# Optimization experiments

Hardware: AMD Instinct MI355X
Metric: run time of the kernel (lower is better)

The kernel has to match this reference:

```python
import jax, jax.numpy as jnp
import numpy as np

B, N, ZDIM = 8, 2048, 128
NPOINTS = 32
BN_EPS = 1e-5


def setup_inputs() -> dict:
    key = jax.random.key(0)
    ks = iter(jax.random.split(key, 64))

    def w(shape, s=0.05):
        return jax.random.normal(next(ks), shape, jnp.float32) * s

    inp = {"x": jax.random.normal(next(ks), (B, N, 3), jnp.float32)}
    inp.update(dict(
        w1=w((128, 3)), b1=w((128,)),
        w2=w((128, 128)), b2=w((128,)),
        w3=w((256, 128)), b3=w((256,)),
        w4=w((512, 256)), b4=w((512,)),
        a1_wqk=w((32, 1)), a1_wt=w((128, 128)), a1_bt=w((128,)),
        a2_wqk=w((32, 1)), a2_wt=w((128, 128)), a2_bt=w((128,)),
        a3_wqk=w((64, 1)), a3_wt=w((256, 256)), a3_bt=w((256,)),
        a4_wqk=w((128, 1)), a4_wt=w((512, 512)), a4_bt=w((512,)),
        fc1m_w=w((256, 512)), fc1m_b=w((256,)),
        fc2m_w=w((128, 256)), fc2m_b=w((128,)),
        fc3m_w=w((ZDIM, 128)), fc3m_b=w((ZDIM,)),
        fc1v_w=w((256, 512)), fc1v_b=w((256,)),
        fc2v_w=w((128, 256)), fc2v_b=w((128,)),
        fc3v_w=w((1, 128)), fc3v_b=w((1,)),
    ))
    return inp


def bn_cn(h):
    # BatchNorm1d over [B, C, N] features (training-mode batch stats, affine=identity at init)
    m = h.mean(axis=(0, 2), keepdims=True)
    v = h.var(axis=(0, 2), keepdims=True)
    return (h - m) * jax.lax.rsqrt(v + BN_EPS)


def bn_f(h):
    # BatchNorm1d over [B, F]
    m = h.mean(axis=0, keepdims=True)
    v = h.var(axis=0, keepdims=True)
    return (h - m) * jax.lax.rsqrt(v + BN_EPS)


def conv1x1(h, w, b):
    # 1x1 Conv1d: [B,Cin,N] x [Cout,Cin] -> [B,Cout,N]
    return jnp.einsum('oc,bcn->bon', w, h) + b[None, :, None]


def angle_density(xyz):
    # xyz: [B,N,3]; 1 - cosine similarity between all point pairs (computed as GEMM,
    # never materializing the [B,N,N,3] expanded tensors of the torch code)
    xn = xyz / jnp.linalg.norm(xyz, axis=-1, keepdims=True)
    dist = 1.0 - jnp.einsum('bnc,bmc->bnm', xn, xn)  # [B,N,N]
    neg_vals, _ = jax.lax.top_k(-dist, NPOINTS)       # 32 smallest distances
    feat_density = (-neg_vals).mean(axis=-1)          # [B,N]
    inv = 1.0 / feat_density
    return inv / jnp.max(inv)


def density_attn(h, dens, wqk, wt, bt):
    # h: [B,C,N], dens: [B,1,N]; q_conv and k_conv share weights
    q = jnp.einsum('dc,bcn->bdn', wqk, dens)          # [B,D4,N]
    energy = jnp.einsum('bdn,bdm->bnm', q, q)         # [B,N,N]
    attn = jax.nn.softmax(energy, axis=-1)
    attn = attn / (1e-9 + attn.sum(axis=1, keepdims=True))
    x_r = jnp.einsum('bcn,bnm->bcm', h, attn)         # [B,C,N]
    t = conv1x1(h - x_r, wt, bt)
    t = jax.nn.relu(bn_cn(t))
    return h + t


def reference(x, w1, b1, w2, b2, w3, b3, w4, b4,
              a1_wqk, a1_wt, a1_bt, a2_wqk, a2_wt, a2_bt,
              a3_wqk, a3_wt, a3_bt, a4_wqk, a4_wt, a4_bt,
              fc1m_w, fc1m_b, fc2m_w, fc2m_b, fc3m_w, fc3m_b,
              fc1v_w, fc1v_b, fc2v_w, fc2v_b, fc3v_w, fc3v_b):
    dens = angle_density(x)[:, None, :]               # [B,1,N]
    h = jnp.swapaxes(x, 1, 2)                         # [B,3,N]
    h = jax.nn.relu(bn_cn(conv1x1(h, w1, b1)))
    h = density_attn(h, dens, a1_wqk, a1_wt, a1_bt)
    h = jax.nn.relu(bn_cn(conv1x1(h, w2, b2)))
    h = density_attn(h, dens, a2_wqk, a2_wt, a2_bt)
    h = jax.nn.relu(bn_cn(conv1x1(h, w3, b3)))
    h = density_attn(h, dens, a3_wqk, a3_wt, a3_bt)
    h = bn_cn(conv1x1(h, w4, b4))                     # no relu on conv4 (matches source)
    h = density_attn(h, dens, a4_wqk, a4_wt, a4_bt)
    g = jnp.max(h, axis=2)                            # [B,512] global max pool

    u = jax.nn.relu(bn_f(g @ fc1m_w.T + fc1m_b))
    u = jax.nn.relu(bn_f(u @ fc2m_w.T + fc2m_b))
    u = u @ fc3m_w.T + fc3m_b
    u = u / jnp.linalg.norm(u, axis=-1, keepdims=True)

    k = jax.nn.relu(bn_f(g @ fc1v_w.T + fc1v_b))
    k = jax.nn.relu(bn_f(k @ fc2v_w.T + fc2v_b))
    k = k @ fc3v_w.T + fc3v_b
    k = jax.nn.softplus(k) + 1.0
    return (u, k)
```

## Files before the change

kernel.cpp:

```cpp
#include <hip/hip_runtime.h>
#include <cfloat>
#include <cmath>

constexpr int NB = 8;
constexpr int NP = 2048;
constexpr int NK = 11;

typedef __attribute__((ext_vector_type(4))) float f32x4;
typedef __attribute__((ext_vector_type(8))) short bf16x8;
#define MFMA16(a, b, c) __builtin_amdgcn_mfma_f32_16x16x32_bf16(a, b, c, 0, 0, 0)

__device__ inline ushort f2bf(float f) {
  union { float f; unsigned u; } v; v.f = f;
  unsigned r = v.u + 0x7FFFu + ((v.u >> 16) & 1u);
  return (ushort)(r >> 16);
}
__device__ inline unsigned pk2bf(float a, float b) {
  return (unsigned)f2bf(a) | ((unsigned)f2bf(b) << 16);
}

__device__ inline int dpp_half_sum_i32(int c) {
  c += __builtin_amdgcn_update_dpp(0, c, 0x111, 0xf, 0xf, true);
  c += __builtin_amdgcn_update_dpp(0, c, 0x112, 0xf, 0xf, true);
  c += __builtin_amdgcn_update_dpp(0, c, 0x114, 0xf, 0xf, true);
  c += __builtin_amdgcn_update_dpp(0, c, 0x118, 0xf, 0xf, true);
  c += __builtin_amdgcn_update_dpp(0, c, 0x142, 0xf, 0xf, true);
  return c;
}

__global__ void k_prep(const float* __restrict__ x, float* __restrict__ xn, float* __restrict__ xt) {
  int i = blockIdx.x * blockDim.x + threadIdx.x;
  if (i >= NB * NP) return;
  int b = i >> 11, n = i & (NP - 1);
  float a0 = x[i * 3 + 0], a1 = x[i * 3 + 1], a2 = x[i * 3 + 2];
  float rn = rsqrtf(a0 * a0 + a1 * a1 + a2 * a2);
  xn[i * 3 + 0] = a0 * rn; xn[i * 3 + 1] = a1 * rn; xn[i * 3 + 2] = a2 * rn;
  float* xb = xt + (size_t)b * 3 * NP;
  xb[0 * NP + n] = a0; xb[1 * NP + n] = a1; xb[2 * NP + n] = a2;
}

__global__ void k_zero1(float* p) { if (threadIdx.x == 0) p[0] = 0.f; }

__global__ __launch_bounds__(512, 1) void k_density(const float* __restrict__ xn,
                                                    float* __restrict__ inv,
                                                    int* __restrict__ maxinv) {
  __shared__ float sx[NP], sy[NP], sz[NP];
  int t = threadIdx.x;
  int w = t >> 6, lane = t & 63, half = lane >> 5, sl = lane & 31;
  int row0 = blockIdx.x * 16;
  int b = row0 >> 11;
  const float4* xb4 = (const float4*)(xn + (size_t)b * NP * 3);
  {
    float4 a = xb4[t * 3 + 0], c4 = xb4[t * 3 + 1], e4 = xb4[t * 3 + 2];
    int p = t * 4;
    sx[p + 0] = a.x;  sy[p + 0] = a.y;  sz[p + 0] = a.z;
    sx[p + 1] = a.w;  sy[p + 1] = c4.x; sz[p + 1] = c4.y;
    sx[p + 2] = c4.z; sy[p + 2] = c4.w; sz[p + 2] = e4.x;
    sx[p + 3] = e4.y; sy[p + 3] = e4.z; sz[p + 3] = e4.w;
  }
  __syncthreads();
  int row = row0 + w * 2 + half;
  int n = row & (NP - 1);
  float px = sx[n], py = sy[n], pz = sz[n];
  float d[64];
  float mn = FLT_MAX, mx = -FLT_MAX;
  #pragma unroll
  for (int k = 0; k < 64; ++k) {
    int m = sl + (k << 5);
    float v = 1.0f - (px * sx[m] + py * sy[m] + pz * sz[m]);
    d[k] = v;
    mn = fminf(mn, v); mx = fmaxf(mx, v);
  }
  #pragma unroll
  for (int off = 16; off; off >>= 1) {
    mn = fminf(mn, __shfl_xor(mn, off));
    mx = fminf(mx, __shfl_xor(mx, off));
  }
  float lo = mn, hi = mx + 1e-6f;
  int baddr = (half ? 63 : 31) << 2;
  for (int it = 0; it < 7; ++it) {
    float dd = hi - lo;
    float t1 = lo + 0.25f * dd, t2 = lo + 0.5f * dd, t3 = lo + 0.75f * dd;
    int c12 = 0, c3 = 0;
    #pragma unroll
    for (int k = 0; k < 64; ++k) {
      float v = d[k];
      c12 += (v < t1 ? 1 : 0) + (v < t2 ? 65536 : 0);
      c3  += (v < t3 ? 1 : 0);
    }
    c12 = dpp_half_sum_i32(c12);
    c3  = dpp_half_sum_i32(c3);
    c12 = __builtin_amdgcn_ds_bpermute(baddr, c12);
    c3  = __builtin_amdgcn_ds_bpermute(baddr, c3);
    int c1 = c12 & 0xFFFF, c2 = (int)(((unsigned)c12) >> 16);
    bool le3 = c3 <= 32, le2 = c2 <= 32, le1 = c1 <= 32;
    float nlo = le3 ? t3 : (le2 ? t2 : (le1 ? t1 : lo));
    float nhi = le3 ? hi : (le2 ? t3 : (le1 ? t2 : t1));
    lo = nlo; hi = nhi;
  }
  {
    float tt = 0.5f * (lo + hi);
    int c = 0;
    #pragma unroll
    for (int k = 0; k < 64; ++k) c += (d[k] < tt) ? 1 : 0;
    c = dpp_half_sum_i32(c);
    c = __builtin_amdgcn_ds_bpermute(baddr, c);
    bool le = c <= 32;
    lo = le ? tt : lo;
  }
  float s = 0.f; int c = 0;
  #pragma unroll
  for (int k = 0; k < 64; ++k) {
    bool p = d[k] < lo;
    s += p ? d[k] : 0.f;
    c += p ? 1 : 0;
  }
  c = dpp_half_sum_i32(c);
  int ctot = __builtin_amdgcn_ds_bpermute(baddr, c);
  #pragma unroll
  for (int off = 16; off; off >>= 1) s += __shfl_xor(s, off);
  float sum = s + (float)(32 - ctot) * lo;
  if (sl == 0) {
    float iv = 32.0f / sum;
    inv[row] = iv;
    atomicMax(maxinv, __float_as_int(iv));
  }
}

__global__ void k_scale(float* __restrict__ dens, const float* __restrict__ maxinv) {
  int i = blockIdx.x * 256 + threadIdx.x;
  if (i < NB * NP) dens[i] *= (1.0f / maxinv[0]);
}

__global__ __launch_bounds__(256) void k_attn_small(const float* __restrict__ dens,
                                                    const float* __restrict__ wqk, int D,
                                                    float* __restrict__ coef_out,
                                                    float* __restrict__ rinv,
                                                    float* __restrict__ cinv) {
  int b = blockIdx.x, t = threadIdx.x, w = t >> 6, lane = t & 63;
  float sv = 0.f;
  for (int i = lane; i < D; i += 64) sv += wqk[i] * wqk[i];
  #pragma unroll
  for (int off = 32; off; off >>= 1) sv += __shfl_xor(sv, off);
  float coef[NK];
  coef[0] = 1.f;
  {
    float cc = 1.f;
    #pragma unroll
    for (int k = 1; k < NK; ++k) { cc *= sv / (float)k; coef[k] = cc; }
  }
  if (b == 0 && t == 0) {
    for (int k = 0; k < NK; ++k) coef_out[k] = coef[k];
  }
  const float* db = dens + b * NP;
  float d[8], r[8];
  *(float4*)&d[0] = *(const float4*)(db + t * 8);
  *(float4*)&d[4] = *(const float4*)(db + t * 8 + 4);
  __shared__ float part[NK][4];
  float q[NK];
  {
    float acc[NK];
    #pragma unroll
    for (int k = 0; k < NK; ++k) acc[k] = 0.f;
    #pragma unroll
    for (int e = 0; e < 8; ++e) {
      float p = 1.f;
      #pragma unroll
      for (int k = 0; k < NK; ++k) { acc[k] += p; p *= d[e]; }
    }
    #pragma unroll
    for (int k = 0; k < NK; ++k) {
      float a = acc[k];
      #pragma unroll
      for (int off = 32; off; off >>= 1) a += __shfl_xor(a, off);
      if (lane == 0) part[k][w] = a;
    }
    __syncthreads();
    #pragma unroll
    for (int k = 0; k < NK; ++k)
      q[k] = coef[k] * ((part[k][0] + part[k][1]) + (part[k][2] + part[k][3]));
    __syncthreads();
  }
  #pragma unroll
  for (int e = 0; e < 8; ++e) {
    float poly = q[NK - 1];
    #pragma unroll
    for (int k = NK - 2; k >= 0; --k) poly = poly * d[e] + q[k];
    r[e] = 1.0f / poly;
  }
  *(float4*)(rinv + b * NP + t * 8)     = *(float4*)&r[0];
  *(float4*)(rinv + b * NP + t * 8 + 4) = *(float4*)&r[4];
  {
    float acc[NK];
    #pragma unroll
    for (int k = 0; k < NK; ++k) acc[k] = 0.f;
    #pragma unroll
    for (int e = 0; e < 8; ++e) {
      float p = r[e];
      #pragma unroll
      for (int k = 0; k < NK; ++k) { acc[k] += p; p *= d[e]; }
    }
    #pragma unroll
    for (int k = 0; k < NK; ++k) {
      float a = acc[k];
      #pragma unroll
      for (int off = 32; off; off >>= 1) a += __shfl_xor(a, off);
      if (lane == 0) part[k][w] = a;
    }
    __syncthreads();
    #pragma unroll
    for (int k = 0; k < NK; ++k)
      q[k] = coef[k] * ((part[k][0] + part[k][1]) + (part[k][2] + part[k][3]));
  }
  #pragma unroll
  for (int e = 0; e < 8; ++e) {
    float poly = q[NK - 1];
    #pragma unroll
    for (int k = NK - 2; k >= 0; --k) poly = poly * d[e] + q[k];
    r[e] = 1.0f / (poly + 1e-9f);
  }
  *(float4*)(cinv + b * NP + t * 8)     = *(float4*)&r[0];
  *(float4*)(cinv + b * NP + t * 8 + 4) = *(float4*)&r[4];
}

__global__ __launch_bounds__(256) void k_xrP(const float* __restrict__ H, float* __restrict__ U,
                                             const float* __restrict__ dens,
                                             const float* __restrict__ rinv,
                                             const float* __restrict__ cinv,
                                             const float* __restrict__ coef, int C) {
  int b = blockIdx.y, c = blockIdx.x, t = threadIdx.x, w = t >> 6, lane = t & 63;
  const float* Hc = H + ((size_t)b * C + c) * NP;
  float* Uc = U + ((size_t)b * C + c) * NP;
  const float* db = dens + b * NP;
  const float* rb = rinv + b * NP;
  const float* cb = cinv + b * NP;
  float h[8], d[8], r[8], cv[8];
  *(float4*)&h[0] = *(const float4*)(Hc + t * 8);
  *(float4*)&h[4] = *(const float4*)(Hc + t * 8 + 4);
  *(float4*)&d[0] = *(const float4*)(db + t * 8);
  *(float4*)&d[4] = *(const float4*)(db + t * 8 + 4);
  *(float4*)&r[0] = *(const float4*)(rb + t * 8);
  *(float4*)&r[4] = *(const float4*)(rb + t * 8 + 4);
  *(float4*)&cv[0] = *(const float4*)(cb + t * 8);
  *(float4*)&cv[4] = *(const float4*)(cb + t * 8 + 4);
  float acc[NK];
  #pragma unroll
  for (int k = 0; k < NK; ++k) acc[k] = 0.f;
  #pragma unroll
  for (int e = 0; e < 8; ++e) {
    float p = h[e] * r[e];
    #pragma unroll
    for (int k = 0; k < NK; ++k) { acc[k] += p; p *= d[e]; }
  }
  __shared__ float part[NK][4];
  #pragma unroll
  for (int k = 0; k < NK; ++k) {
    float a = acc[k];
    #pragma unroll
    for (int off = 32; off; off >>= 1) a += __shfl_xor(a, off);
    if (lane == 0) part[k][w] = a;
  }
  __syncthreads();
  float q[NK];
  #pragma unroll
  for (int k = 0; k < NK; ++k)
    q[k] = coef[k] * ((part[k][0] + part[k][1]) + (part[k][2] + part[k][3]));
  float u[8];
  #pragma unroll
  for (int e = 0; e < 8; ++e) {
    float poly = q[NK - 1];
    #pragma unroll
    for (int k = NK - 2; k >= 0; --k) poly = poly * d[e] + q[k];
    u[e] = h[e] - cv[e] * poly;
  }
  *(float4*)(Uc + t * 8)     = *(float4*)&u[0];
  *(float4*)(Uc + t * 8 + 4) = *(float4*)&u[4];
}

constexpr int LDA = 72;

__global__ __launch_bounds__(256) void k_gemm_mfma(const float* __restrict__ W,
                                                   const float* __restrict__ IN,
                                                   const float* __restrict__ bias,
                                                   float* __restrict__ OUT,
                                                   int Cin, int Cout) {
  int b = blockIdx.z, n0 = blockIdx.x * 128, o0 = blockIdx.y * 128;
  int tid = threadIdx.x, lane = tid & 63, w = tid >> 6;
  int wr = w >> 1, wc = w & 1;
  const float* Ib = IN + (size_t)b * Cin * NP;
  float* Ob = OUT + (size_t)b * Cout * NP;
  __shared__ ushort Asm[128 * LDA];
  __shared__ ushort Bsm[128 * LDA];
  f32x4 acc[4][4];
  #pragma unroll
  for (int i = 0; i < 4; ++i)
    #pragma unroll
    for (int j = 0; j < 4; ++j) acc[i][j] = (f32x4)(0.0f);

  int row = tid >> 1, half = tid & 1;
  int csub = tid & 63, q = tid >> 6;
  for (int cc0 = 0; cc0 < Cin; cc0 += 64) {
    __syncthreads();
    {
      const float* src = W + (size_t)(o0 + row) * Cin + cc0 + half * 32;
      unsigned* dst = (unsigned*)(Asm + row * LDA + half * 32);
      #pragma unroll
      for (int i = 0; i < 8; ++i) {
        float4 v = *(const float4*)(src + i * 4);
        dst[i * 2 + 0] = pk2bf(v.x, v.y);
        dst[i * 2 + 1] = pk2bf(v.z, v.w);
      }
      const float* isrc = Ib + (size_t)(cc0 + csub) * NP + n0 + q * 32;
      #pragma unroll
      for (int i = 0; i < 8; ++i) {
        float4 v = *(const float4*)(isrc + i * 4);
        ushort* bd = Bsm + (q * 32 + i * 4) * LDA + csub;
        bd[0]       = f2bf(v.x);
        bd[LDA]     = f2bf(v.y);
        bd[2 * LDA] = f2bf(v.z);
        bd[3 * LDA] = f2bf(v.w);
      }
    }
    __syncthreads();
    #pragma unroll
    for (int kk = 0; kk < 64; kk += 32) {
      bf16x8 af[4], bfr[4];
      #pragma unroll
      for (int i = 0; i < 4; ++i) {
        af[i]  = *(const bf16x8*)(Asm + (wr * 64 + i * 16 + (lane & 15)) * LDA + kk + (lane >> 4) * 8);
        bfr[i] = *(const bf16x8*)(Bsm + (wc * 64 + i * 16 + (lane & 15)) * LDA + kk + (lane >> 4) * 8);
      }
      #pragma unroll
      for (int i = 0; i < 4; ++i)
        #pragma unroll
        for (int j = 0; j < 4; ++j)
          acc[i][j] = MFMA16(af[i], bfr[j], acc[i][j]);
    }
  }
  #pragma unroll
  for (int i = 0; i < 4; ++i) {
    #pragma unroll
    for (int r = 0; r < 4; ++r) {
      int o = o0 + wr * 64 + i * 16 + (lane >> 4) * 4 + r;
      float bv = bias[o];
      #pragma unroll
      for (int j = 0; j < 4; ++j) {
        int n = n0 + wc * 64 + j * 16 + (lane & 15);
        Ob[(size_t)o * NP + n] = acc[i][j][r] + bv;
      }
    }
  }
}

__global__ __launch_bounds__(256) void k_gemm(const float* __restrict__ W,
                                              const float* __restrict__ IN,
                                              const float* __restrict__ bias,
                                              float* __restrict__ OUT,
                                              int Cin, int Cout) {
  int b = blockIdx.z;
  int n0 = blockIdx.x * 64;
  int o0 = blockIdx.y * 64;
  int tid = threadIdx.x;
  int tx = tid & 15, ty = tid >> 4;
  const float* Ib = IN + (size_t)b * Cin * NP;
  float* Ob = OUT + (size_t)b * Cout * NP;
  __shared__ float Wt[64][65];
  __shared__ float It[64][65];
  float acc[4][4] = {};
  for (int c0 = 0; c0 < Cin; c0 += 64) {
    __syncthreads();
    {
      int ci = tid & 63, ob4 = tid >> 6;
      bool cv = (c0 + ci) < Cin;
      #pragma unroll
      for (int k = 0; k < 16; ++k) {
        int oi = ob4 + (k << 2);
        Wt[ci][oi] = cv ? W[(size_t)(o0 + oi) * Cin + c0 + ci] : 0.f;
      }
      int ni = tid & 63, cb4 = tid >> 6;
      #pragma unroll
      for (int k = 0; k < 16; ++k) {
        int ci2 = cb4 + (k << 2);
        It[ci2][ni] = (c0 + ci2) < Cin ? Ib[(size_t)(c0 + ci2) * NP + n0 + ni] : 0.f;
      }
    }
    __syncthreads();
    #pragma unroll 4
    for (int ci = 0; ci < 64; ++ci) {
      float a0 = Wt[ci][ty * 4 + 0], a1 = Wt[ci][ty * 4 + 1], a2 = Wt[ci][ty * 4 + 2], a3 = Wt[ci][ty * 4 + 3];
      float b0 = It[ci][tx * 4 + 0], b1 = It[ci][tx * 4 + 1], b2 = It[ci][tx * 4 + 2], b3 = It[ci][tx * 4 + 3];
      acc[0][0] += a0 * b0; acc[0][1] += a0 * b1; acc[0][2] += a0 * b2; acc[0][3] += a0 * b3;
      acc[1][0] += a1 * b0; acc[1][1] += a1 * b1; acc[1][2] += a1 * b2; acc[1][3] += a1 * b3;
      acc[2][0] += a2 * b0; acc[2][1] += a2 * b1; acc[2][2] += a2 * b2; acc[2][3] += a2 * b3;
      acc[3][0] += a3 * b0; acc[3][1] += a3 * b1; acc[3][2] += a3 * b2; acc[3][3] += a3 * b3;
    }
  }
  #pragma unroll
  for (int i = 0; i < 4; ++i) {
    int o = o0 + ty * 4 + i;
    float bv = bias[o];
    #pragma unroll
    for (int j = 0; j < 4; ++j) {
      int n = n0 + tx * 4 + j;
      Ob[(size_t)o * NP + n] = acc[i][j] + bv;
    }
  }
}

__global__ __launch_bounds__(256) void k_bn(const float* __restrict__ T, float* __restrict__ H,
                                            int C, int relu, int acc, int pool,
                                            float* __restrict__ gout) {
  int c = blockIdx.x, t = threadIdx.x, w = t >> 6, lane = t & 63;
  float4 v[16];
  float s = 0.f, s2 = 0.f;
  #pragma unroll
  for (int b = 0; b < NB; ++b) {
    const float4* p = (const float4*)(T + ((size_t)b * C + c) * NP);
    #pragma unroll
    for (int i = 0; i < 2; ++i) {
      float4 x = p[t + i * 256];
      v[b * 2 + i] = x;
      s += (x.x + x.y) + (x.z + x.w);
      s2 += (x.x * x.x + x.y * x.y) + (x.z * x.z + x.w * x.w);
    }
  }
  #pragma unroll
  for (int off = 32; off; off >>= 1) { s += __shfl_xor(s, off); s2 += __shfl_xor(s2, off); }
  __shared__ float ps[4], ps2[4];
  if (lane == 0) { ps[w] = s; ps2[w] = s2; }
  __syncthreads();
  float ts = (ps[0] + ps[1]) + (ps[2] + ps[3]);
  float ts2 = (ps2[0] + ps2[1]) + (ps2[2] + ps2[3]);
  float m = ts * (1.0f / (NB * NP));
  float var = ts2 * (1.0f / (NB * NP)) - m * m;
  float is = rsqrtf(var + 1e-5f);
  float bmax[NB];
  #pragma unroll
  for (int b = 0; b < NB; ++b) bmax[b] = -FLT_MAX;
  #pragma unroll
  for (int b = 0; b < NB; ++b) {
    float4* hp = (float4*)(H + ((size_t)b * C + c) * NP);
    #pragma unroll
    for (int i = 0; i < 2; ++i) {
      float4 x = v[b * 2 + i];
      x.x = (x.x - m) * is; x.y = (x.y - m) * is; x.z = (x.z - m) * is; x.w = (x.w - m) * is;
      if (relu) {
        x.x = fmaxf(x.x, 0.f); x.y = fmaxf(x.y, 0.f); x.z = fmaxf(x.z, 0.f); x.w = fmaxf(x.w, 0.f);
      }
      if (acc) {
        float4 h = hp[t + i * 256];
        x.x += h.x; x.y += h.y; x.z += h.z; x.w += h.w;
      }
      hp[t + i * 256] = x;
      if (pool) bmax[b] = fmaxf(bmax[b], fmaxf(fmaxf(x.x, x.y), fmaxf(x.z, x.w)));
    }
  }
  if (pool) {
    __shared__ float pm[4][NB];
    #pragma unroll
    for (int b = 0; b < NB; ++b) {
      float m2 = bmax[b];
      #pragma unroll
      for (int off = 32; off; off >>= 1) m2 = fmaxf(m2, __shfl_xor(m2, off));
      if (lane == 0) pm[w][b] = m2;
    }
    __syncthreads();
    if (t < NB) {
      float m2 = fmaxf(fmaxf(pm[0][t], pm[1][t]), fmaxf(pm[2][t], pm[3][t]));
      gout[t * C + c] = m2;
    }
  }
}

__global__ __launch_bounds__(256) void k_head(const float* __restrict__ g,
    const float* __restrict__ f1mw, const float* __restrict__ f1mb,
    const float* __restrict__ f2mw, const float* __restrict__ f2mb,
    const float* __restrict__ f3mw, const float* __restrict__ f3mb,
    const float* __restrict__ f1vw, const float* __restrict__ f1vb,
    const float* __restrict__ f2vw, const float* __restrict__ f2vb,
    const float* __restrict__ f3vw, const float* __restrict__ f3vb,
    float* __restrict__ out) {
  bool vpath = (blockIdx.x == 1);
  const float* w1 = vpath ? f1vw : f1mw;
  const float* c1 = vpath ? f1vb : f1mb;
  const float* w2 = vpath ? f2vw : f2mw;
  const float* c2 = vpath ? f2vb : f2mb;
  __shared__ float gg[NB * 512];
  __shared__ float a1[NB * 256];
  __shared__ float a2[NB * 128];
  __shared__ float zz[NB * 128];
  __shared__ float nrm[NB];
  int t = threadIdx.x;
  for (int i = t; i < NB * 512; i += 256) gg[i] = g[i];
  __syncthreads();
  float o[NB];
  {
    #pragma unroll
    for (int b = 0; b < NB; ++b) o[b] = c1[t];
    const float* wr = w1 + (size_t)t * 512;
    for (int j = 0; j < 512; ++j) {
      float w = wr[j];
      #pragma unroll
      for (int b = 0; b < NB; ++b) o[b] += gg[b * 512 + j] * w;
    }
    float mean = 0.f;
    #pragma unroll
    for (int b = 0; b < NB; ++b) mean += o[b];
    mean *= (1.0f / NB);
    float var = 0.f;
    #pragma unroll
    for (int b = 0; b < NB; ++b) { float d = o[b] - mean; var += d * d; }
    var *= (1.0f / NB);
    float is = rsqrtf(var + 1e-5f);
    #pragma unroll
    for (int b = 0; b < NB; ++b) a1[b * 256 + t] = fmaxf((o[b] - mean) * is, 0.f);
  }
  __syncthreads();
  if (t < 128) {
    #pragma unroll
    for (int b = 0; b < NB; ++b) o[b] = c2[t];
    const float* wr = w2 + (size_t)t * 256;
    for (int j = 0; j < 256; ++j) {
      float w = wr[j];
      #pragma unroll
      for (int b = 0; b < NB; ++b) o[b] += a1[b * 256 + j] * w;
    }
    float mean = 0.f;
    #pragma unroll
    for (int b = 0; b < NB; ++b) mean += o[b];
    mean *= (1.0f / NB);
    float var = 0.f;
    #pragma unroll
    for (int b = 0; b < NB; ++b) { float d = o[b] - mean; var += d * d; }
    var *= (1.0f / NB);
    float is = rsqrtf(var + 1e-5f);
    #pragma unroll
    for (int b = 0; b < NB; ++b) a2[b * 128 + t] = fmaxf((o[b] - mean) * is, 0.f);
  }
  __syncthreads();
  if (!vpath) {
    if (t < 128) {
      const float* wr = f3mw + (size_t)t * 128;
      for (int b = 0; b < NB; ++b) {
        float s = f3mb[t];
        for (int j = 0; j < 128; ++j) s += a2[b * 128 + j] * wr[j];
        zz[b * 128 + t] = s;
      }
    }
    __syncthreads();
    if (t < NB) {
      float s = 0.f;
      for (int j = 0; j < 128; ++j) { float v = zz[t * 128 + j]; s += v * v; }
      nrm[t] = sqrtf(s);
    }
    __syncthreads();
    if (t < 128) {
      for (int b = 0; b < NB; ++b) out[b * 128 + t] = zz[b * 128 + t] / nrm[b];
    }
  } else {
    if (t < NB) {
      float s = f3vb[0];
      for (int j = 0; j < 128; ++j) s += a2[t * 128 + j] * f3vw[j];
      float sp = (s > 20.f) ? s : log1pf(expf(s));
      out[NB * 128 + t] = sp + 1.0f;
    }
  }
}

extern "C" void kernel_launch(void* const* d_in, const int* in_sizes, int n_in,
                              void* d_out, int out_size, void* d_ws, size_t ws_size,
                              hipStream_t stream) {
  const float* x  = (const float*)d_in[0];
  const float* w1 = (const float*)d_in[1];
  const float* b1 = (const float*)d_in[2];
  const float* w2 = (const float*)d_in[3];
  const float* b2 = (const float*)d_in[4];
  const float* w3 = (const float*)d_in[5];
  const float* b3 = (const float*)d_in[6];
  const float* w4 = (const float*)d_in[7];
  const float* b4 = (const float*)d_in[8];
  const float* a_wqk[4] = {(const float*)d_in[9],  (const float*)d_in[12], (const float*)d_in[15], (const float*)d_in[18]};
  const float* a_wt[4]  = {(const float*)d_in[10], (const float*)d_in[13], (const float*)d_in[16], (const float*)d_in[19]};
  const float* a_bt[4]  = {(const float*)d_in[11], (const float*)d_in[14], (const float*)d_in[17], (const float*)d_in[20]};
  int a_D[4] = {in_sizes[9], in_sizes[12], in_sizes[15], in_sizes[18]};
  const float* f1mw = (const float*)d_in[21]; const float* f1mb = (const float*)d_in[22];
  const float* f2mw = (const float*)d_in[23]; const float* f2mb = (const float*)d_in[24];
  const float* f3mw = (const float*)d_in[25]; const float* f3mb = (const float*)d_in[26];
  const float* f1vw = (const float*)d_in[27]; const float* f1vb = (const float*)d_in[28];
  const float* f2vw = (const float*)d_in[29]; const float* f2vb = (const float*)d_in[30];
  const float* f3vw = (const float*)d_in[31]; const float* f3vb = (const float*)d_in[32];
  float* out = (float*)d_out;

  float* ws = (float*)d_ws;
  float* xn     = ws; ws += (size_t)NB * NP * 3;
  float* dens   = ws; ws += NB * NP;
  float* maxinv = ws; ws += 16;
  float* coef   = ws; ws += 16;
  float* rinv   = ws; ws += NB * NP;
  float* cinv   = ws; ws += NB * NP;
  float* g      = ws; ws += NB * 512;
  float* Hb     = ws; ws += (size_t)NB * 512 * NP;
  float* Ub     = ws; ws += (size_t)NB * 512 * NP;
  float* Tb     = ws; ws += (size_t)NB * 512 * NP;

  k_prep<<<NB * NP / 256, 256, 0, stream>>>(x, xn, Ub);
  k_zero1<<<1, 64, 0, stream>>>(maxinv);
  k_density<<<NB * NP / 16, 512, 0, stream>>>(xn, dens, (int*)maxinv);
  k_scale<<<NB * NP / 256, 256, 0, stream>>>(dens, maxinv);

  auto conv = [&](const float* W, const float* bias, const float* IN, int Cin, int Cout, bool relu) {
    if (Cin < 64)
      k_gemm<<<dim3(NP / 64, Cout / 64, NB), 256, 0, stream>>>(W, IN, bias, Tb, Cin, Cout);
    else
      k_gemm_mfma<<<dim3(NP / 128, Cout / 128, NB), 256, 0, stream>>>(W, IN, bias, Tb, Cin, Cout);
    k_bn<<<Cout, 256, 0, stream>>>(Tb, Hb, Cout, relu ? 1 : 0, 0, 0, g);
  };
  auto attn = [&](int li, int C) {
    k_attn_small<<<NB, 256, 0, stream>>>(dens, a_wqk[li], a_D[li], coef, rinv, cinv);
    k_xrP<<<dim3(C, NB), 256, 0, stream>>>(Hb, Ub, dens, rinv, cinv, coef, C);
    k_gemm_mfma<<<dim3(NP / 128, C / 128, NB), 256, 0, stream>>>(a_wt[li], Ub, a_bt[li], Tb, C, C);
    k_bn<<<C, 256, 0, stream>>>(Tb, Hb, C, 1, 1, (li == 3) ? 1 : 0, g);
  };

  conv(w1, b1, Ub, 3, 128, true);
  attn(0, 128);
  conv(w2, b2, Hb, 128, 128, true);
  attn(1, 128);
  conv(w3, b3, Hb, 128, 256, true);
  attn(2, 256);
  conv(w4, b4, Hb, 256, 512, false);
  attn(3, 512);

  k_head<<<2, 256, 0, stream>>>(g, f1mw, f1mb, f2mw, f2mb, f3mw, f3mb,
                                f1vw, f1vb, f2vw, f2vb, f3vw, f3vb, out);
}
```

Measured before the change: 467.8 us.

## Store density distances as fp16 in LDS and bisect on integer bit patterns

The density top-k kernel now gives each row a full wavefront, keeps its 2048 distances as packed fp16 in shared memory instead of 64 fp32 registers per lane, and bisects on the integer fp16 bit patterns using whole-wave DPP reductions. The aim is to cut register pressure so more blocks fit per CU, and to make the threshold search exact over a discrete range. The cost is more LDS traffic per search pass, twice as many blocks, and fp16 rounding of the distances, which may change the selected threshold and sum slightly.

```diff
diff --git a/kernel.cpp b/kernel.cpp
--- a/kernel.cpp
+++ b/kernel.cpp
@@ -1,4 +1,5 @@
 #include <hip/hip_runtime.h>
+#include <hip/hip_fp16.h>
 #include <cfloat>
 #include <cmath>
 
@@ -19,13 +20,14 @@
   return (unsigned)f2bf(a) | ((unsigned)f2bf(b) << 16);
 }
 
-__device__ inline int dpp_half_sum_i32(int c) {
+__device__ inline int dpp_wave_sum_i32(int c) {
   c += __builtin_amdgcn_update_dpp(0, c, 0x111, 0xf, 0xf, true);
   c += __builtin_amdgcn_update_dpp(0, c, 0x112, 0xf, 0xf, true);
   c += __builtin_amdgcn_update_dpp(0, c, 0x114, 0xf, 0xf, true);
   c += __builtin_amdgcn_update_dpp(0, c, 0x118, 0xf, 0xf, true);
   c += __builtin_amdgcn_update_dpp(0, c, 0x142, 0xf, 0xf, true);
-  return c;
+  c += __builtin_amdgcn_update_dpp(0, c, 0x143, 0xf, 0xf, true);
+  return __builtin_amdgcn_readlane(c, 63);
 }
 
 __global__ void k_prep(const float* __restrict__ x, float* __restrict__ xn, float* __restrict__ xt) {
@@ -41,13 +43,14 @@
 
 __global__ void k_zero1(float* p) { if (threadIdx.x == 0) p[0] = 0.f; }
 
-__global__ __launch_bounds__(512, 1) void k_density(const float* __restrict__ xn,
-                                                    float* __restrict__ inv,
-                                                    int* __restrict__ maxinv) {
+__global__ __launch_bounds__(512) void k_density(const float* __restrict__ xn,
+                                                 float* __restrict__ inv,
+                                                 int* __restrict__ maxinv) {
   __shared__ float sx[NP], sy[NP], sz[NP];
+  __shared__ uint2 dq[8][NP / 4];
   int t = threadIdx.x;
-  int w = t >> 6, lane = t & 63, half = lane >> 5, sl = lane & 31;
-  int row0 = blockIdx.x * 16;
+  int w = t >> 6, lane = t & 63;
+  int row0 = blockIdx.x * 8;
   int b = row0 >> 11;
   const float4* xb4 = (const float4*)(xn + (size_t)b * NP * 3);
   {
@@ -59,68 +62,82 @@
     sx[p + 3] = e4.y; sy[p + 3] = e4.z; sz[p + 3] = e4.w;
   }
   __syncthreads();
-  int row = row0 + w * 2 + half;
+  int row = row0 + w;
   int n = row & (NP - 1);
   float px = sx[n], py = sy[n], pz = sz[n];
-  float d[64];
-  float mn = FLT_MAX, mx = -FLT_MAX;
-  #pragma unroll
-  for (int k = 0; k < 64; ++k) {
-    int m = sl + (k << 5);
-    float v = 1.0f - (px * sx[m] + py * sy[m] + pz * sz[m]);
-    d[k] = v;
-    mn = fminf(mn, v); mx = fmaxf(mx, v);
-  }
-  #pragma unroll
-  for (int off = 16; off; off >>= 1) {
-    mn = fminf(mn, __shfl_xor(mn, off));
-    mx = fminf(mx, __shfl_xor(mx, off));
-  }
-  float lo = mn, hi = mx + 1e-6f;
-  int baddr = (half ? 63 : 31) << 2;
-  for (int it = 0; it < 7; ++it) {
-    float dd = hi - lo;
-    float t1 = lo + 0.25f * dd, t2 = lo + 0.5f * dd, t3 = lo + 0.75f * dd;
+  uint2* drow = dq[w];
+  int mni = 0xFFFF, mxi = 0;
+  #pragma unroll
+  for (int k4 = 0; k4 < 8; ++k4) {
+    unsigned u[4];
+    #pragma unroll
+    for (int i = 0; i < 4; ++i) {
+      int m = lane + ((k4 * 4 + i) << 6);
+      float v = fmaxf(1.0f - (px * sx[m] + py * sy[m] + pz * sz[m]), 0.0f);
+      u[i] = (unsigned)__half_as_ushort(__float2half(v));
+      mni = min(mni, (int)u[i]); mxi = max(mxi, (int)u[i]);
+    }
+    drow[(k4 << 6) + lane] = make_uint2(u[0] | (u[1] << 16), u[2] | (u[3] << 16));
+  }
+  #pragma unroll
+  for (int off = 32; off; off >>= 1) {
+    mni = min(mni, __shfl_xor(mni, off));
+    mxi = min(mxi, __shfl_xor(mxi, off));
+  }
+  int lo = mni, hi = mxi + 1;
+  #pragma unroll
+  for (int it = 0; it < 8; ++it) {
+    int dd = hi - lo;
+    int t1 = lo + (dd >> 2), t2 = lo + (dd >> 1), t3 = lo + dd - (dd >> 2);
     int c12 = 0, c3 = 0;
     #pragma unroll
-    for (int k = 0; k < 64; ++k) {
-      float v = d[k];
-      c12 += (v < t1 ? 1 : 0) + (v < t2 ? 65536 : 0);
-      c3  += (v < t3 ? 1 : 0);
-    }
-    c12 = dpp_half_sum_i32(c12);
-    c3  = dpp_half_sum_i32(c3);
-    c12 = __builtin_amdgcn_ds_bpermute(baddr, c12);
-    c3  = __builtin_amdgcn_ds_bpermute(baddr, c3);
+    for (int k4 = 0; k4 < 8; ++k4) {
+      uint2 pp = drow[(k4 << 6) + lane];
+      int e0 = (int)(pp.x & 0xFFFF), e1 = (int)(pp.x >> 16);
+      int e2 = (int)(pp.y & 0xFFFF), e3 = (int)(pp.y >> 16);
+      int a1 = (e0 < t1 ? 1 : 0) + (e1 < t1 ? 1 : 0) + (e2 < t1 ? 1 : 0) + (e3 < t1 ? 1 : 0);
+      int a2 = (e0 < t2 ? 1 : 0) + (e1 < t2 ? 1 : 0) + (e2 < t2 ? 1 : 0) + (e3 < t2 ? 1 : 0);
+      c12 += a1 + (a2 << 16);
+      c3  += (e0 < t3 ? 1 : 0) + (e1 < t3 ? 1 : 0) + (e2 < t3 ? 1 : 0) + (e3 < t3 ? 1 : 0);
+    }
+    c12 = dpp_wave_sum_i32(c12);
+    c3  = dpp_wave_sum_i32(c3);
     int c1 = c12 & 0xFFFF, c2 = (int)(((unsigned)c12) >> 16);
     bool le3 = c3 <= 32, le2 = c2 <= 32, le1 = c1 <= 32;
-    float nlo = le3 ? t3 : (le2 ? t2 : (le1 ? t1 : lo));
-    float nhi = le3 ? hi : (le2 ? t3 : (le1 ? t2 : t1));
+    int nlo = le3 ? t3 : (le2 ? t2 : (le1 ? t1 : lo));
+    int nhi = le3 ? hi : (le2 ? t3 : (le1 ? t2 : t1));
     lo = nlo; hi = nhi;
   }
-  {
-    float tt = 0.5f * (lo + hi);
+  #pragma unroll
+  for (int it = 0; it < 2; ++it) {
+    int tt = lo + ((hi - lo) >> 1);
     int c = 0;
     #pragma unroll
-    for (int k = 0; k < 64; ++k) c += (d[k] < tt) ? 1 : 0;
-    c = dpp_half_sum_i32(c);
-    c = __builtin_amdgcn_ds_bpermute(baddr, c);
-    bool le = c <= 32;
-    lo = le ? tt : lo;
+    for (int k4 = 0; k4 < 8; ++k4) {
+      uint2 pp = drow[(k4 << 6) + lane];
+      c += ((int)(pp.x & 0xFFFF) < tt ? 1 : 0) + ((int)(pp.x >> 16) < tt ? 1 : 0)
+         + ((int)(pp.y & 0xFFFF) < tt ? 1 : 0) + ((int)(pp.y >> 16) < tt ? 1 : 0);
+    }
+    c = dpp_wave_sum_i32(c);
+    if (c <= 32) lo = tt; else hi = tt;
   }
   float s = 0.f; int c = 0;
   #pragma unroll
-  for (int k = 0; k < 64; ++k) {
-    bool p = d[k] < lo;
-    s += p ? d[k] : 0.f;
-    c += p ? 1 : 0;
-  }
-  c = dpp_half_sum_i32(c);
-  int ctot = __builtin_amdgcn_ds_bpermute(baddr, c);
-  #pragma unroll
-  for (int off = 16; off; off >>= 1) s += __shfl_xor(s, off);
-  float sum = s + (float)(32 - ctot) * lo;
-  if (sl == 0) {
+  for (int k4 = 0; k4 < 8; ++k4) {
+    uint2 pp = drow[(k4 << 6) + lane];
+    int e[4] = {(int)(pp.x & 0xFFFF), (int)(pp.x >> 16), (int)(pp.y & 0xFFFF), (int)(pp.y >> 16)};
+    #pragma unroll
+    for (int i = 0; i < 4; ++i) {
+      bool p = e[i] < lo;
+      s += p ? __half2float(__ushort_as_half((ushort)e[i])) : 0.f;
+      c += p ? 1 : 0;
+    }
+  }
+  int ctot = dpp_wave_sum_i32(c);
+  #pragma unroll
+  for (int off = 32; off; off >>= 1) s += __shfl_xor(s, off);
+  float sum = s + (float)(32 - ctot) * __half2float(__ushort_as_half((ushort)lo));
+  if (lane == 0) {
     float iv = 32.0f / sum;
     inv[row] = iv;
     atomicMax(maxinv, __float_as_int(iv));
@@ -605,7 +622,7 @@
 
   k_prep<<<NB * NP / 256, 256, 0, stream>>>(x, xn, Ub);
   k_zero1<<<1, 64, 0, stream>>>(maxinv);
-  k_density<<<NB * NP / 16, 512, 0, stream>>>(xn, dens, (int*)maxinv);
+  k_density<<<NB * NP / 8, 512, 0, stream>>>(xn, dens, (int*)maxinv);
   k_scale<<<NB * NP / 256, 256, 0, stream>>>(dens, maxinv);
 
   auto conv = [&](const float* W, const float* bias, const float* IN, int Cin, int Cout, bool relu) {
```

Measured after the change: 554.2 us. +18.5%, slower.

## Fuse per-batch attention normalizer into k_xrP and simplify density bisection

Applied to the files above, without the earlier changes.

Removes the separate k_attn_small launch by recomputing the per-batch row and column normalizers inside every k_xrP block, so the rinv/cinv/coef buffers are no longer written or read. This saves four kernel launches and the global round-trips, at the cost of redundant polynomial reductions in every channel block (C times per batch). Separately, the top-k threshold search replaces 7 quaternary bisection steps (three thresholds each) plus one refinement with 18 plain binary bisection steps, which trades fewer compares per step for more sequential steps.

```diff
diff --git a/kernel.cpp b/kernel.cpp
--- a/kernel.cpp
+++ b/kernel.cpp
@@ -78,35 +78,16 @@
   }
   float lo = mn, hi = mx + 1e-6f;
   int baddr = (half ? 63 : 31) << 2;
-  for (int it = 0; it < 7; ++it) {
-    float dd = hi - lo;
-    float t1 = lo + 0.25f * dd, t2 = lo + 0.5f * dd, t3 = lo + 0.75f * dd;
-    int c12 = 0, c3 = 0;
-    #pragma unroll
-    for (int k = 0; k < 64; ++k) {
-      float v = d[k];
-      c12 += (v < t1 ? 1 : 0) + (v < t2 ? 65536 : 0);
-      c3  += (v < t3 ? 1 : 0);
-    }
-    c12 = dpp_half_sum_i32(c12);
-    c3  = dpp_half_sum_i32(c3);
-    c12 = __builtin_amdgcn_ds_bpermute(baddr, c12);
-    c3  = __builtin_amdgcn_ds_bpermute(baddr, c3);
-    int c1 = c12 & 0xFFFF, c2 = (int)(((unsigned)c12) >> 16);
-    bool le3 = c3 <= 32, le2 = c2 <= 32, le1 = c1 <= 32;
-    float nlo = le3 ? t3 : (le2 ? t2 : (le1 ? t1 : lo));
-    float nhi = le3 ? hi : (le2 ? t3 : (le1 ? t2 : t1));
-    lo = nlo; hi = nhi;
-  }
-  {
+  for (int it = 0; it < 18; ++it) {
     float tt = 0.5f * (lo + hi);
     int c = 0;
     #pragma unroll
     for (int k = 0; k < 64; ++k) c += (d[k] < tt) ? 1 : 0;
     c = dpp_half_sum_i32(c);
-    c = __builtin_amdgcn_ds_bpermute(baddr, c);
-    bool le = c <= 32;
+    int ct = __builtin_amdgcn_ds_bpermute(baddr, c);
+    bool le = ct <= 32;
     lo = le ? tt : lo;
+    hi = le ? hi : tt;
   }
   float s = 0.f; int c = 0;
   #pragma unroll
@@ -132,12 +113,10 @@
   if (i < NB * NP) dens[i] *= (1.0f / maxinv[0]);
 }
 
-__global__ __launch_bounds__(256) void k_attn_small(const float* __restrict__ dens,
-                                                    const float* __restrict__ wqk, int D,
-                                                    float* __restrict__ coef_out,
-                                                    float* __restrict__ rinv,
-                                                    float* __restrict__ cinv) {
-  int b = blockIdx.x, t = threadIdx.x, w = t >> 6, lane = t & 63;
+__global__ __launch_bounds__(256) void k_xrP(const float* __restrict__ H, float* __restrict__ U,
+                                             const float* __restrict__ dens,
+                                             const float* __restrict__ wqk, int D, int C) {
+  int b = blockIdx.y, c = blockIdx.x, t = threadIdx.x, w = t >> 6, lane = t & 63;
   float sv = 0.f;
   for (int i = lane; i < D; i += 64) sv += wqk[i] * wqk[i];
   #pragma unroll
@@ -149,101 +128,71 @@
     #pragma unroll
     for (int k = 1; k < NK; ++k) { cc *= sv / (float)k; coef[k] = cc; }
   }
-  if (b == 0 && t == 0) {
-    for (int k = 0; k < NK; ++k) coef_out[k] = coef[k];
-  }
-  const float* db = dens + b * NP;
-  float d[8], r[8];
-  *(float4*)&d[0] = *(const float4*)(db + t * 8);
-  *(float4*)&d[4] = *(const float4*)(db + t * 8 + 4);
-  __shared__ float part[NK][4];
-  float q[NK];
-  {
-    float acc[NK];
-    #pragma unroll
-    for (int k = 0; k < NK; ++k) acc[k] = 0.f;
-    #pragma unroll
-    for (int e = 0; e < 8; ++e) {
-      float p = 1.f;
-      #pragma unroll
-      for (int k = 0; k < NK; ++k) { acc[k] += p; p *= d[e]; }
-    }
-    #pragma unroll
-    for (int k = 0; k < NK; ++k) {
-      float a = acc[k];
-      #pragma unroll
-      for (int off = 32; off; off >>= 1) a += __shfl_xor(a, off);
-      if (lane == 0) part[k][w] = a;
-    }
-    __syncthreads();
-    #pragma unroll
-    for (int k = 0; k < NK; ++k)
-      q[k] = coef[k] * ((part[k][0] + part[k][1]) + (part[k][2] + part[k][3]));
-    __syncthreads();
-  }
-  #pragma unroll
-  for (int e = 0; e < 8; ++e) {
-    float poly = q[NK - 1];
-    #pragma unroll
-    for (int k = NK - 2; k >= 0; --k) poly = poly * d[e] + q[k];
-    r[e] = 1.0f / poly;
-  }
-  *(float4*)(rinv + b * NP + t * 8)     = *(float4*)&r[0];
-  *(float4*)(rinv + b * NP + t * 8 + 4) = *(float4*)&r[4];
-  {
-    float acc[NK];
-    #pragma unroll
-    for (int k = 0; k < NK; ++k) acc[k] = 0.f;
-    #pragma unroll
-    for (int e = 0; e < 8; ++e) {
-      float p = r[e];
-      #pragma unroll
-      for (int k = 0; k < NK; ++k) { acc[k] += p; p *= d[e]; }
-    }
-    #pragma unroll
-    for (int k = 0; k < NK; ++k) {
-      float a = acc[k];
-      #pragma unroll
-      for (int off = 32; off; off >>= 1) a += __shfl_xor(a, off);
-      if (lane == 0) part[k][w] = a;
-    }
-    __syncthreads();
-    #pragma unroll
-    for (int k = 0; k < NK; ++k)
-      q[k] = coef[k] * ((part[k][0] + part[k][1]) + (part[k][2] + part[k][3]));
-  }
-  #pragma unroll
-  for (int e = 0; e < 8; ++e) {
-    float poly = q[NK - 1];
-    #pragma unroll
-    for (int k = NK - 2; k >= 0; --k) poly = poly * d[e] + q[k];
-    r[e] = 1.0f / (poly + 1e-9f);
-  }
-  *(float4*)(cinv + b * NP + t * 8)     = *(float4*)&r[0];
-  *(float4*)(cinv + b * NP + t * 8 + 4) = *(float4*)&r[4];
-}
-
-__global__ __launch_bounds__(256) void k_xrP(const float* __restrict__ H, float* __restrict__ U,
-                                             const float* __restrict__ dens,
-                                             const float* __restrict__ rinv,
-                                             const float* __restrict__ cinv,
-                                             const float* __restrict__ coef, int C) {
-  int b = blockIdx.y, c = blockIdx.x, t = threadIdx.x, w = t >> 6, lane = t & 63;
   const float* Hc = H + ((size_t)b * C + c) * NP;
   float* Uc = U + ((size_t)b * C + c) * NP;
   const float* db = dens + b * NP;
-  const float* rb = rinv + b * NP;
-  const float* cb = cinv + b * NP;
-  float h[8], d[8], r[8], cv[8];
+  float h[8], d[8], r[8];
   *(float4*)&h[0] = *(const float4*)(Hc + t * 8);
   *(float4*)&h[4] = *(const float4*)(Hc + t * 8 + 4);
   *(float4*)&d[0] = *(const float4*)(db + t * 8);
   *(float4*)&d[4] = *(const float4*)(db + t * 8 + 4);
-  *(float4*)&r[0] = *(const float4*)(rb + t * 8);
-  *(float4*)&r[4] = *(const float4*)(rb + t * 8 + 4);
-  *(float4*)&cv[0] = *(const float4*)(cb + t * 8);
-  *(float4*)&cv[4] = *(const float4*)(cb + t * 8 + 4);
-  float acc[NK];
+  __shared__ float part[NK][4];
+  float q[NK], acc[NK];
+  #pragma unroll
+  for (int k = 0; k < NK; ++k) acc[k] = 0.f;
+  #pragma unroll
+  for (int e = 0; e < 8; ++e) {
+    float p = 1.f;
+    #pragma unroll
+    for (int k = 0; k < NK; ++k) { acc[k] += p; p *= d[e]; }
+  }
+  #pragma unroll
+  for (int k = 0; k < NK; ++k) {
+    float a = acc[k];
+    #pragma unroll
+    for (int off = 32; off; off >>= 1) a += __shfl_xor(a, off);
+    if (lane == 0) part[k][w] = a;
+  }
+  __syncthreads();
+  #pragma unroll
+  for (int k = 0; k < NK; ++k)
+    q[k] = coef[k] * ((part[k][0] + part[k][1]) + (part[k][2] + part[k][3]));
+  __syncthreads();
+  #pragma unroll
+  for (int e = 0; e < 8; ++e) {
+    float poly = q[NK - 1];
+    #pragma unroll
+    for (int k = NK - 2; k >= 0; --k) poly = poly * d[e] + q[k];
+    r[e] = 1.0f / poly;
+  }
+  #pragma unroll
+  for (int k = 0; k < NK; ++k) acc[k] = 0.f;
+  #pragma unroll
+  for (int e = 0; e < 8; ++e) {
+    float p = r[e];
+    #pragma unroll
+    for (int k = 0; k < NK; ++k) { acc[k] += p; p *= d[e]; }
+  }
+  #pragma unroll
+  for (int k = 0; k < NK; ++k) {
+    float a = acc[k];
+    #pragma unroll
+    for (int off = 32; off; off >>= 1) a += __shfl_xor(a, off);
+    if (lane == 0) part[k][w] = a;
+  }
+  __syncthreads();
+  #pragma unroll
+  for (int k = 0; k < NK; ++k)
+    q[k] = coef[k] * ((part[k][0] + part[k][1]) + (part[k][2] + part[k][3]));
+  __syncthreads();
+  float cv[8];
+  #pragma unroll
+  for (int e = 0; e < 8; ++e) {
+    float poly = q[NK - 1];
+    #pragma unroll
+    for (int k = NK - 2; k >= 0; --k) poly = poly * d[e] + q[k];
+    cv[e] = 1.0f / (poly + 1e-9f);
+  }
   #pragma unroll
   for (int k = 0; k < NK; ++k) acc[k] = 0.f;
   #pragma unroll
@@ -252,7 +201,6 @@
     #pragma unroll
     for (int k = 0; k < NK; ++k) { acc[k] += p; p *= d[e]; }
   }
-  __shared__ float part[NK][4];
   #pragma unroll
   for (int k = 0; k < NK; ++k) {
     float a = acc[k];
@@ -261,7 +209,6 @@
     if (lane == 0) part[k][w] = a;
   }
   __syncthreads();
-  float q[NK];
   #pragma unroll
   for (int k = 0; k < NK; ++k)
     q[k] = coef[k] * ((part[k][0] + part[k][1]) + (part[k][2] + part[k][3]));
@@ -595,9 +542,6 @@
   float* xn     = ws; ws += (size_t)NB * NP * 3;
   float* dens   = ws; ws += NB * NP;
   float* maxinv = ws; ws += 16;
-  float* coef   = ws; ws += 16;
-  float* rinv   = ws; ws += NB * NP;
-  float* cinv   = ws; ws += NB * NP;
   float* g      = ws; ws += NB * 512;
   float* Hb     = ws; ws += (size_t)NB * 512 * NP;
   float* Ub     = ws; ws += (size_t)NB * 512 * NP;
@@ -616,8 +560,7 @@
     k_bn<<<Cout, 256, 0, stream>>>(Tb, Hb, Cout, relu ? 1 : 0, 0, 0, g);
   };
   auto attn = [&](int li, int C) {
-    k_attn_small<<<NB, 256, 0, stream>>>(dens, a_wqk[li], a_D[li], coef, rinv, cinv);
-    k_xrP<<<dim3(C, NB), 256, 0, stream>>>(Hb, Ub, dens, rinv, cinv, coef, C);
+    k_xrP<<<dim3(C, NB), 256, 0, stream>>>(Hb, Ub, dens, a_wqk[li], a_D[li], C);
     k_gemm_mfma<<<dim3(NP / 128, C / 128, NB), 256, 0, stream>>>(a_wt[li], Ub, a_bt[li], Tb, C, C);
     k_bn<<<C, 256, 0, stream>>>(Tb, Hb, C, 1, 1, (li == 3) ? 1 : 0, g);
   };
```

After: 503.8 us. 1.08x slower.

## Fuse batchnorm with attention projection kernel and simplify density bisection

Applied to the files above, without the earlier changes.

Merges the batchnorm kernel after each conv with the density-attention x·r·P projection, so the normalized activations stay in registers and the separate k_xrP kernel no longer re-reads H from global memory. k_attn_small is moved ahead of the conv GEMM so its coefficients are ready for the fused kernel. The density top-k threshold search swaps the 7-round 4-way split for 18 rounds of plain bisection, which costs more counting passes but does one comparison per element per round. The fused kernel runs the per-batch reductions serially with a barrier each iteration, which lowers parallelism per channel.

```diff
diff --git a/kernel.cpp b/kernel.cpp
--- a/kernel.cpp
+++ b/kernel.cpp
@@ -78,35 +78,16 @@
   }
   float lo = mn, hi = mx + 1e-6f;
   int baddr = (half ? 63 : 31) << 2;
-  for (int it = 0; it < 7; ++it) {
-    float dd = hi - lo;
-    float t1 = lo + 0.25f * dd, t2 = lo + 0.5f * dd, t3 = lo + 0.75f * dd;
-    int c12 = 0, c3 = 0;
-    #pragma unroll
-    for (int k = 0; k < 64; ++k) {
-      float v = d[k];
-      c12 += (v < t1 ? 1 : 0) + (v < t2 ? 65536 : 0);
-      c3  += (v < t3 ? 1 : 0);
-    }
-    c12 = dpp_half_sum_i32(c12);
-    c3  = dpp_half_sum_i32(c3);
-    c12 = __builtin_amdgcn_ds_bpermute(baddr, c12);
-    c3  = __builtin_amdgcn_ds_bpermute(baddr, c3);
-    int c1 = c12 & 0xFFFF, c2 = (int)(((unsigned)c12) >> 16);
-    bool le3 = c3 <= 32, le2 = c2 <= 32, le1 = c1 <= 32;
-    float nlo = le3 ? t3 : (le2 ? t2 : (le1 ? t1 : lo));
-    float nhi = le3 ? hi : (le2 ? t3 : (le1 ? t2 : t1));
-    lo = nlo; hi = nhi;
-  }
-  {
+  for (int it = 0; it < 18; ++it) {
     float tt = 0.5f * (lo + hi);
     int c = 0;
     #pragma unroll
     for (int k = 0; k < 64; ++k) c += (d[k] < tt) ? 1 : 0;
     c = dpp_half_sum_i32(c);
-    c = __builtin_amdgcn_ds_bpermute(baddr, c);
-    bool le = c <= 32;
+    int ct = __builtin_amdgcn_ds_bpermute(baddr, c);
+    bool le = ct <= 32;
     lo = le ? tt : lo;
+    hi = le ? hi : tt;
   }
   float s = 0.f; int c = 0;
   #pragma unroll
@@ -221,60 +202,6 @@
   }
   *(float4*)(cinv + b * NP + t * 8)     = *(float4*)&r[0];
   *(float4*)(cinv + b * NP + t * 8 + 4) = *(float4*)&r[4];
-}
-
-__global__ __launch_bounds__(256) void k_xrP(const float* __restrict__ H, float* __restrict__ U,
-                                             const float* __restrict__ dens,
-                                             const float* __restrict__ rinv,
-                                             const float* __restrict__ cinv,
-                                             const float* __restrict__ coef, int C) {
-  int b = blockIdx.y, c = blockIdx.x, t = threadIdx.x, w = t >> 6, lane = t & 63;
-  const float* Hc = H + ((size_t)b * C + c) * NP;
-  float* Uc = U + ((size_t)b * C + c) * NP;
-  const float* db = dens + b * NP;
-  const float* rb = rinv + b * NP;
-  const float* cb = cinv + b * NP;
-  float h[8], d[8], r[8], cv[8];
-  *(float4*)&h[0] = *(const float4*)(Hc + t * 8);
-  *(float4*)&h[4] = *(const float4*)(Hc + t * 8 + 4);
-  *(float4*)&d[0] = *(const float4*)(db + t * 8);
-  *(float4*)&d[4] = *(const float4*)(db + t * 8 + 4);
-  *(float4*)&r[0] = *(const float4*)(rb + t * 8);
-  *(float4*)&r[4] = *(const float4*)(rb + t * 8 + 4);
-  *(float4*)&cv[0] = *(const float4*)(cb + t * 8);
-  *(float4*)&cv[4] = *(const float4*)(cb + t * 8 + 4);
-  float acc[NK];
-  #pragma unroll
-  for (int k = 0; k < NK; ++k) acc[k] = 0.f;
-  #pragma unroll
-  for (int e = 0; e < 8; ++e) {
-    float p = h[e] * r[e];
-    #pragma unroll
-    for (int k = 0; k < NK; ++k) { acc[k] += p; p *= d[e]; }
-  }
-  __shared__ float part[NK][4];
-  #pragma unroll
-  for (int k = 0; k < NK; ++k) {
-    float a = acc[k];
-    #pragma unroll
-    for (int off = 32; off; off >>= 1) a += __shfl_xor(a, off);
-    if (lane == 0) part[k][w] = a;
-  }
-  __syncthreads();
-  float q[NK];
-  #pragma unroll
-  for (int k = 0; k < NK; ++k)
-    q[k] = coef[k] * ((part[k][0] + part[k][1]) + (part[k][2] + part[k][3]));
-  float u[8];
-  #pragma unroll
-  for (int e = 0; e < 8; ++e) {
-    float poly = q[NK - 1];
-    #pragma unroll
-    for (int k = NK - 2; k >= 0; --k) poly = poly * d[e] + q[k];
-    u[e] = h[e] - cv[e] * poly;
-  }
-  *(float4*)(Uc + t * 8)     = *(float4*)&u[0];
-  *(float4*)(Uc + t * 8 + 4) = *(float4*)&u[4];
 }
 
 constexpr int LDA = 72;
@@ -404,6 +331,103 @@
       int n = n0 + tx * 4 + j;
       Ob[(size_t)o * NP + n] = acc[i][j] + bv;
     }
+  }
+}
+
+__global__ __launch_bounds__(256) void k_bnxr(const float* __restrict__ T, float* __restrict__ H,
+                                              float* __restrict__ U,
+                                              const float* __restrict__ dens,
+                                              const float* __restrict__ rinv,
+                                              const float* __restrict__ cinv,
+                                              const float* __restrict__ coef_g,
+                                              int C, int relu) {
+  int c = blockIdx.x, t = threadIdx.x, w = t >> 6, lane = t & 63;
+  float4 v[16];
+  float s = 0.f, s2 = 0.f;
+  #pragma unroll
+  for (int b = 0; b < NB; ++b) {
+    const float4* p = (const float4*)(T + ((size_t)b * C + c) * NP);
+    #pragma unroll
+    for (int i = 0; i < 2; ++i) {
+      float4 x = p[t + i * 256];
+      v[b * 2 + i] = x;
+      s += (x.x + x.y) + (x.z + x.w);
+      s2 += (x.x * x.x + x.y * x.y) + (x.z * x.z + x.w * x.w);
+    }
+  }
+  #pragma unroll
+  for (int off = 32; off; off >>= 1) { s += __shfl_xor(s, off); s2 += __shfl_xor(s2, off); }
+  __shared__ float ps[4], ps2[4];
+  if (lane == 0) { ps[w] = s; ps2[w] = s2; }
+  __syncthreads();
+  float ts = (ps[0] + ps[1]) + (ps[2] + ps[3]);
+  float ts2 = (ps2[0] + ps2[1]) + (ps2[2] + ps2[3]);
+  float m = ts * (1.0f / (NB * NP));
+  float var = ts2 * (1.0f / (NB * NP)) - m * m;
+  float is = rsqrtf(var + 1e-5f);
+  #pragma unroll
+  for (int b = 0; b < NB; ++b) {
+    float4* hp = (float4*)(H + ((size_t)b * C + c) * NP);
+    #pragma unroll
+    for (int i = 0; i < 2; ++i) {
+      float4 x = v[b * 2 + i];
+      x.x = (x.x - m) * is; x.y = (x.y - m) * is; x.z = (x.z - m) * is; x.w = (x.w - m) * is;
+      if (relu) {
+        x.x = fmaxf(x.x, 0.f); x.y = fmaxf(x.y, 0.f); x.z = fmaxf(x.z, 0.f); x.w = fmaxf(x.w, 0.f);
+      }
+      hp[t + i * 256] = x;
+      v[b * 2 + i] = x;
+    }
+  }
+  float coef[NK];
+  #pragma unroll
+  for (int k = 0; k < NK; ++k) coef[k] = coef_g[k];
+  __shared__ float part[NK][4];
+  for (int b = 0; b < NB; ++b) {
+    float4 dA = *(const float4*)(dens + b * NP + 4 * t);
+    float4 dB = *(const float4*)(dens + b * NP + 1024 + 4 * t);
+    float4 rA = *(const float4*)(rinv + b * NP + 4 * t);
+    float4 rB = *(const float4*)(rinv + b * NP + 1024 + 4 * t);
+    float4 cA = *(const float4*)(cinv + b * NP + 4 * t);
+    float4 cB = *(const float4*)(cinv + b * NP + 1024 + 4 * t);
+    float d8[8] = {dA.x, dA.y, dA.z, dA.w, dB.x, dB.y, dB.z, dB.w};
+    float r8[8] = {rA.x, rA.y, rA.z, rA.w, rB.x, rB.y, rB.z, rB.w};
+    float c8[8] = {cA.x, cA.y, cA.z, cA.w, cB.x, cB.y, cB.z, cB.w};
+    float h8[8] = {v[b*2].x, v[b*2].y, v[b*2].z, v[b*2].w,
+                   v[b*2+1].x, v[b*2+1].y, v[b*2+1].z, v[b*2+1].w};
+    float acc[NK];
+    #pragma unroll
+    for (int k = 0; k < NK; ++k) acc[k] = 0.f;
+    #pragma unroll
+    for (int e = 0; e < 8; ++e) {
+      float p = h8[e] * r8[e];
+      #pragma unroll
+      for (int k = 0; k < NK; ++k) { acc[k] += p; p *= d8[e]; }
+    }
+    #pragma unroll
+    for (int k = 0; k < NK; ++k) {
+      float a = acc[k];
+      #pragma unroll
+      for (int off = 32; off; off >>= 1) a += __shfl_xor(a, off);
+      if (lane == 0) part[k][w] = a;
+    }
+    __syncthreads();
+    float q[NK];
+    #pragma unroll
+    for (int k = 0; k < NK; ++k)
+      q[k] = coef[k] * ((part[k][0] + part[k][1]) + (part[k][2] + part[k][3]));
+    float u8[8];
+    #pragma unroll
+    for (int e = 0; e < 8; ++e) {
+      float poly = q[NK - 1];
+      #pragma unroll
+      for (int k = NK - 2; k >= 0; --k) poly = poly * d8[e] + q[k];
+      u8[e] = h8[e] - c8[e] * poly;
+    }
+    float* Uc = U + ((size_t)b * C + c) * NP;
+    *(float4*)(Uc + 4 * t)        = make_float4(u8[0], u8[1], u8[2], u8[3]);
+    *(float4*)(Uc + 1024 + 4 * t) = make_float4(u8[4], u8[5], u8[6], u8[7]);
+    __syncthreads();
   }
 }
 
@@ -608,28 +632,22 @@
   k_density<<<NB * NP / 16, 512, 0, stream>>>(xn, dens, (int*)maxinv);
   k_scale<<<NB * NP / 256, 256, 0, stream>>>(dens, maxinv);
 
-  auto conv = [&](const float* W, const float* bias, const float* IN, int Cin, int Cout, bool relu) {
+  auto stage = [&](int li, const float* W, const float* bias, const float* IN,
+                   int Cin, int Cout, bool relu) {
+    k_attn_small<<<NB, 256, 0, stream>>>(dens, a_wqk[li], a_D[li], coef, rinv, cinv);
     if (Cin < 64)
       k_gemm<<<dim3(NP / 64, Cout / 64, NB), 256, 0, stream>>>(W, IN, bias, Tb, Cin, Cout);
     else
       k_gemm_mfma<<<dim3(NP / 128, Cout / 128, NB), 256, 0, stream>>>(W, IN, bias, Tb, Cin, Cout);
-    k_bn<<<Cout, 256, 0, stream>>>(Tb, Hb, Cout, relu ? 1 : 0, 0, 0, g);
+    k_bnxr<<<Cout, 256, 0, stream>>>(Tb, Hb, Ub, dens, rinv, cinv, coef, Cout, relu ? 1 : 0);
+    k_gemm_mfma<<<dim3(NP / 128, Cout / 128, NB), 256, 0, stream>>>(a_wt[li], Ub, a_bt[li], Tb, Cout, Cout);
+    k_bn<<<Cout, 256, 0, stream>>>(Tb, Hb, Cout, 1, 1, (li == 3) ? 1 : 0, g);
   };
-  auto attn = [&](int li, int C) {
-    k_attn_small<<<NB, 256, 0, stream>>>(dens, a_wqk[li], a_D[li], coef, rinv, cinv);
-    k_xrP<<<dim3(C, NB), 256, 0, stream>>>(Hb, Ub, dens, rinv, cinv, coef, C);
-    k_gemm_mfma<<<dim3(NP / 128, C / 128, NB), 256, 0, stream>>>(a_wt[li], Ub, a_bt[li], Tb, C, C);
-    k_bn<<<C, 256, 0, stream>>>(Tb, Hb, C, 1, 1, (li == 3) ? 1 : 0, g);
-  };
-
-  conv(w1, b1, Ub, 3, 128, true);
-  attn(0, 128);
-  conv(w2, b2, Hb, 128, 128, true);
-  attn(1, 128);
-  conv(w3, b3, Hb, 128, 256, true);
-  attn(2, 256);
-  conv(w4, b4, Hb, 256, 512, false);
-  attn(3, 512);
+
+  stage(0, w1, b1, Ub, 3, 128, true);
+  stage(1, w2, b2, Hb, 128, 128, true);
+  stage(2, w3, b3, Hb, 128, 256, true);
+  stage(3, w4, b4, Hb, 256, 512, false);
 
   k_head<<<2, 256, 0, stream>>>(g, f1mw, f1mb, f2mw, f2mb, f3mw, f3mb,
                                 f1vw, f1vb, f2vw, f2vb, f3vw, f3vb, out);
```

Result: slower. 548.8 us (+17.3%).
